# Optimization experiments

Measured on AMD Instinct MI355X. Metric: run time of the kernel, lower is better.

## Reference

```python
import math
import jax, jax.numpy as jnp
import numpy as np

EMBED_DIM = 128
NUM_HEADS = 2
B, N = 4096, 32  # batch of fully-connected ally graphs, N allies each (self-edges included)


def sparsemax(z, axis):
    """Sparsemax (Martins & Astudillo 2016) along `axis`."""
    K = z.shape[axis]
    z_sorted = -jnp.sort(-z, axis=axis)  # descending
    z_cumsum = jnp.cumsum(z_sorted, axis=axis)
    shape = [1] * z.ndim
    shape[axis] = K
    k = jnp.arange(1, K + 1, dtype=z.dtype).reshape(shape)
    support = (1.0 + k * z_sorted) > z_cumsum
    k_sup = jnp.sum(support.astype(z.dtype), axis=axis, keepdims=True)
    tau = (jnp.sum(jnp.where(support, z_sorted, 0.0), axis=axis, keepdims=True) - 1.0) / k_sup
    return jnp.maximum(z - tau, 0.0)


def setup_inputs() -> dict:
    key = jax.random.key(0)
    k1, k2, k3, k4 = jax.random.split(key, 4)
    D, H = EMBED_DIM, NUM_HEADS
    node_feature = jax.random.normal(k1, (B, N, D), dtype=jnp.float32)
    scale = 1.0 / math.sqrt(D)
    WK = jax.random.normal(k2, (D, H * D), dtype=jnp.float32) * scale
    WV = jax.random.normal(k3, (D, H * D), dtype=jnp.float32) * scale
    WQ = jax.random.normal(k4, (D, H * D), dtype=jnp.float32) * scale
    return {"node_feature": node_feature, "WK": WK, "WV": WV, "WQ": WQ}


def reference(node_feature, WK, WV, WQ):
    D, H = EMBED_DIM, NUM_HEADS
    x = node_feature  # [B, N, D]
    # per-node projections; Linear(D, H*D) reshaped to (H, D) as in torch .view
    k = (x @ WK).reshape(B, N, H, D)
    v = (x @ WV).reshape(B, N, H, D)
    q = (x @ WQ).reshape(B, N, H, D)
    # fully connected graph: node i attends over mailbox of all nodes j in same graph
    score = jnp.einsum("bihd,bjhd->bijh", q, k) / math.sqrt(D * H)  # [B, N(i), N(j), H]
    w = sparsemax(score, axis=2)  # sparsemax over neighbor (mailbox) dim
    out = jnp.einsum("bijh,bjhd->bihd", w, v)  # weighted reduction
    out = out.mean(axis=2)  # mean over heads -> [B, N, D]
    output = out.reshape(B * N, D)
    # weight padded to max_num_allies (= N here, so no extra padding needed)
    weight = w.reshape(B * N, N, H)
    return output, weight
```

## Files before the change

### kernel.cpp

```cpp
#include <hip/hip_runtime.h>
#include <hip/hip_bf16.h>


#define NG 4096

typedef short bf16x8 __attribute__((ext_vector_type(8)));
typedef float f32x4 __attribute__((ext_vector_type(4)));

__device__ inline short f2bf(float f) {
    __hip_bfloat16 h = __float2bfloat16(f);
    return __builtin_bit_cast(short, h);
}
__device__ inline unsigned pack2(float a, float b) {
    return (unsigned)(unsigned short)f2bf(a) | ((unsigned)(unsigned short)f2bf(b) << 16);
}

__global__ void pack_m_kernel(const float* __restrict__ WQ, const float* __restrict__ WK,
                              short* __restrict__ packed_m) {
    int idx  = blockIdx.x * 256 + threadIdx.x;
    int jj   = idx & 7;
    int lane = (idx >> 3) & 63;
    int s    = (idx >> 9) & 3;
    int mt   = (idx >> 11) & 15;
    int h    = mt >> 3;
    int a    = s * 32 + (lane >> 4) * 8 + jj;
    int bl   = (mt & 7) * 16 + (lane & 15);
    const float4* qa = (const float4*)(WQ + a * 256 + h * 128);
    const float4* kb = (const float4*)(WK + bl * 256 + h * 128);
    float acc = 0.f;
    #pragma unroll 8
    for (int c = 0; c < 32; ++c) {
        float4 q4 = qa[c], k4 = kb[c];
        acc += q4.x * k4.x + q4.y * k4.y + q4.z * k4.z + q4.w * k4.w;
    }
    packed_m[idx] = f2bf(acc * 0.0625f);
}

__global__ void pack_v_kernel(const float* __restrict__ WV, short* __restrict__ packed_v) {
    int idx  = blockIdx.x * 256 + threadIdx.x;
    int jj   = idx & 7;
    int lane = (idx >> 3) & 63;
    int s    = (idx >> 9) & 3;
    int t    = (idx >> 11) & 15;
    int krow = s * 32 + (lane >> 4) * 8 + jj;
    int col  = t * 16 + (lane & 15);
    packed_v[idx] = f2bf(WV[krow * 256 + col]);
}

__global__ __launch_bounds__(256, 3)
void fused_attn_kernel(const float* __restrict__ x, const short* __restrict__ pm,
                       const short* __restrict__ pv, float* __restrict__ out,
                       float* __restrict__ wgt) {
    __shared__ char __align__(16) smem[46592];
    short* t_s  = (short*)smem;
    short* vT_s = (short*)(smem + 16896);
    float* s_s  = (float*)(smem + 37376);

    int b    = blockIdx.x;
    int tid  = threadIdx.x;
    int lane = tid & 63;
    int wave = tid >> 6;
    int lrow = lane & 15;
    int quad = lane >> 4;

    bf16x8 xf[2][4];
    const float* xg = x + (size_t)b * 4096;
    #pragma unroll
    for (int nt = 0; nt < 2; ++nt)
        #pragma unroll
        for (int s = 0; s < 4; ++s) {
            const float* p0 = &xg[(nt * 16 + lrow) * 128 + s * 32 + quad * 8];
            float4 f0 = *(const float4*)p0;
            float4 f1 = *(const float4*)(p0 + 4);
            bf16x8 v;
            v[0]=f2bf(f0.x); v[1]=f2bf(f0.y); v[2]=f2bf(f0.z); v[3]=f2bf(f0.w);
            v[4]=f2bf(f1.x); v[5]=f2bf(f1.y); v[6]=f2bf(f1.z); v[7]=f2bf(f1.w);
            xf[nt][s] = v;
        }

    #pragma unroll
    for (int t = 0; t < 4; ++t) {
        int mt = wave * 4 + t;
        const short* pb = pm + (mt * 4) * 512 + lane * 8;
        bf16x8 wf[4];
        #pragma unroll
        for (int s = 0; s < 4; ++s) wf[s] = *(const bf16x8*)&pb[s * 512];
        f32x4 acc[2] = {{0.f,0.f,0.f,0.f},{0.f,0.f,0.f,0.f}};
        #pragma unroll
        for (int nt = 0; nt < 2; ++nt)
            #pragma unroll
            for (int s = 0; s < 4; ++s)
                acc[nt] = __builtin_amdgcn_mfma_f32_16x16x32_bf16(wf[s], xf[nt][s], acc[nt], 0, 0, 0);
        #pragma unroll
        for (int nt = 0; nt < 2; ++nt) {
            int addr = (nt * 16 + lrow) * 264 + mt * 16 + quad * 4;
            uint2 pk; pk.x = pack2(acc[nt][0], acc[nt][1]); pk.y = pack2(acc[nt][2], acc[nt][3]);
            *(uint2*)&t_s[addr] = pk;
        }
    }
    #pragma unroll
    for (int t = 0; t < 4; ++t) {
        int ntv = wave * 4 + t;
        const short* pb = pv + (ntv * 4) * 512 + lane * 8;
        bf16x8 wf[4];
        #pragma unroll
        for (int s = 0; s < 4; ++s) wf[s] = *(const bf16x8*)&pb[s * 512];
        f32x4 acc[2] = {{0.f,0.f,0.f,0.f},{0.f,0.f,0.f,0.f}};
        #pragma unroll
        for (int mt = 0; mt < 2; ++mt)
            #pragma unroll
            for (int s = 0; s < 4; ++s)
                acc[mt] = __builtin_amdgcn_mfma_f32_16x16x32_bf16(xf[mt][s], wf[s], acc[mt], 0, 0, 0);
        #pragma unroll
        for (int mt = 0; mt < 2; ++mt) {
            int addr = (ntv * 16 + lrow) * 40 + mt * 16 + quad * 4;
            uint2 pk; pk.x = pack2(acc[mt][0], acc[mt][1]); pk.y = pack2(acc[mt][2], acc[mt][3]);
            *(uint2*)&vT_s[addr] = pk;
        }
    }
    __syncthreads();

    #pragma unroll
    for (int tt = 0; tt < 2; ++tt) {
        int ti = wave * 2 + tt;
        int h = ti >> 2, it = (ti >> 1) & 1, jt = ti & 1;
        f32x4 acc = {0.f, 0.f, 0.f, 0.f};
        #pragma unroll
        for (int s = 0; s < 4; ++s) {
            bf16x8 at = *(const bf16x8*)&t_s[(it * 16 + lrow) * 264 + h * 128 + s * 32 + quad * 8];
            acc = __builtin_amdgcn_mfma_f32_16x16x32_bf16(at, xf[jt][s], acc, 0, 0, 0);
        }
        #pragma unroll
        for (int r = 0; r < 4; ++r)
            s_s[(h * 32 + it * 16 + quad * 4 + r) * 36 + jt * 16 + lrow] = acc[r];
    }
    __syncthreads();

    {
        int j  = lane & 31;
        int hh = lane >> 5;
        #pragma unroll
        for (int ii = 0; ii < 8; ++ii) {
            int i   = wave * 8 + ii;
            int row = hh * 32 + i;
            const float* zr = &s_s[row * 36];
            float z[32];
            #pragma unroll
            for (int c = 0; c < 8; ++c) {
                float4 f = *(const float4*)&zr[c * 4];
                z[c*4] = f.x; z[c*4+1] = f.y; z[c*4+2] = f.z; z[c*4+3] = f.w;
            }
            float zj = zr[j];
            float c0 = 0.f, c1 = 0.f, s0 = 0.f, s1 = 0.f;
            #pragma unroll
            for (int l = 0; l < 32; l += 2) {
                bool g0 = z[l]     > zj;
                bool g1 = z[l + 1] > zj;
                c0 += g0 ? 1.f : 0.f;  s0 += g0 ? z[l]     : 0.f;
                c1 += g1 ? 1.f : 0.f;  s1 += g1 ? z[l + 1] : 0.f;
            }
            float rk  = c0 + c1 + 1.f;
            float cum = s0 + s1 + zj;
            float tc  = (cum - 1.f) / rk;
            #pragma unroll
            for (int m = 1; m <= 16; m <<= 1) tc = fmaxf(tc, __shfl_xor(tc, m, 32));
            float w = fmaxf(zj - tc, 0.f);
            ((short*)zr)[j] = f2bf(w);
            float wo = __shfl_xor(w, 32);
            if (lane < 32) {
                float2 v; v.x = w; v.y = wo;
                *(float2*)&wgt[((size_t)b * 32 + i) * 64 + j * 2] = v;
            }
        }
    }
    __syncthreads();

    #pragma unroll
    for (int tt = 0; tt < 4; ++tt) {
        int ti = wave * 4 + tt;
        int it = ti >> 3, dt = ti & 7;
        f32x4 acc = {0.f, 0.f, 0.f, 0.f};
        #pragma unroll
        for (int h = 0; h < 2; ++h) {
            bf16x8 aw = *(const bf16x8*)((short*)&s_s[(h * 32 + it * 16 + lrow) * 36] + quad * 8);
            bf16x8 bv = *(const bf16x8*)&vT_s[(h * 128 + dt * 16 + lrow) * 40 + quad * 8];
            acc = __builtin_amdgcn_mfma_f32_16x16x32_bf16(aw, bv, acc, 0, 0, 0);
        }
        #pragma unroll
        for (int r = 0; r < 4; ++r)
            out[((size_t)b * 32 + it * 16 + quad * 4 + r) * 128 + dt * 16 + lrow] = acc[r] * 0.5f;
    }
}

extern "C" void kernel_launch(void* const* d_in, const int* in_sizes, int n_in,
                              void* d_out, int out_size, void* d_ws, size_t ws_size,
                              hipStream_t stream) {
    const float* x  = (const float*)d_in[0];
    const float* WK = (const float*)d_in[1];
    const float* WV = (const float*)d_in[2];
    const float* WQ = (const float*)d_in[3];
    float* out = (float*)d_out;
    float* wgt = out + (size_t)NG * 32 * 128;
    short* pm = (short*)d_ws;
    short* pv = pm + 32768;

    hipLaunchKernelGGL(pack_m_kernel, dim3(128), dim3(256), 0, stream, WQ, WK, pm);
    hipLaunchKernelGGL(pack_v_kernel, dim3(128), dim3(256), 0, stream, WV, pv);
    hipLaunchKernelGGL(fused_attn_kernel, dim3(NG), dim3(256), 0, stream, x, pm, pv, out, wgt);
}
```

Measured before the change: 205.8 us.

## Alias score buffer onto projection smem to raise occupancy, merge pack kernels

The score buffer now reuses the shared-memory region of the t projection buffer. An extra barrier and register staging of the score accumulators make this aliasing safe. Shared memory per block drops from about 46KB to 37KB, and launch bounds move from 3 to 4 blocks per SIMD so more workgroups can be resident. The two weight-pack kernels are merged into one launch, and the sparsemax mask-sum now uses an FMA. The costs are one extra barrier per block and possible register pressure under the tighter launch bound.

```diff
diff --git a/kernel.cpp b/kernel.cpp
--- a/kernel.cpp
+++ b/kernel.cpp
@@ -15,46 +15,48 @@
     return (unsigned)(unsigned short)f2bf(a) | ((unsigned)(unsigned short)f2bf(b) << 16);
 }
 
-__global__ void pack_m_kernel(const float* __restrict__ WQ, const float* __restrict__ WK,
-                              short* __restrict__ packed_m) {
-    int idx  = blockIdx.x * 256 + threadIdx.x;
-    int jj   = idx & 7;
-    int lane = (idx >> 3) & 63;
-    int s    = (idx >> 9) & 3;
-    int mt   = (idx >> 11) & 15;
-    int h    = mt >> 3;
-    int a    = s * 32 + (lane >> 4) * 8 + jj;
-    int bl   = (mt & 7) * 16 + (lane & 15);
-    const float4* qa = (const float4*)(WQ + a * 256 + h * 128);
-    const float4* kb = (const float4*)(WK + bl * 256 + h * 128);
-    float acc = 0.f;
-    #pragma unroll 8
-    for (int c = 0; c < 32; ++c) {
-        float4 q4 = qa[c], k4 = kb[c];
-        acc += q4.x * k4.x + q4.y * k4.y + q4.z * k4.z + q4.w * k4.w;
-    }
-    packed_m[idx] = f2bf(acc * 0.0625f);
-}
-
-__global__ void pack_v_kernel(const float* __restrict__ WV, short* __restrict__ packed_v) {
-    int idx  = blockIdx.x * 256 + threadIdx.x;
-    int jj   = idx & 7;
-    int lane = (idx >> 3) & 63;
-    int s    = (idx >> 9) & 3;
-    int t    = (idx >> 11) & 15;
-    int krow = s * 32 + (lane >> 4) * 8 + jj;
-    int col  = t * 16 + (lane & 15);
-    packed_v[idx] = f2bf(WV[krow * 256 + col]);
-}
-
-__global__ __launch_bounds__(256, 3)
+__global__ void pack_mv_kernel(const float* __restrict__ WQ, const float* __restrict__ WK,
+                               const float* __restrict__ WV,
+                               short* __restrict__ pm, short* __restrict__ pv) {
+    int gidx = blockIdx.x * 256 + threadIdx.x;
+    if (gidx < 32768) {
+        int idx  = gidx;
+        int jj   = idx & 7;
+        int lane = (idx >> 3) & 63;
+        int s    = (idx >> 9) & 3;
+        int mt   = (idx >> 11) & 15;
+        int h    = mt >> 3;
+        int a    = s * 32 + (lane >> 4) * 8 + jj;
+        int bl   = (mt & 7) * 16 + (lane & 15);
+        const float4* qa = (const float4*)(WQ + a * 256 + h * 128);
+        const float4* kb = (const float4*)(WK + bl * 256 + h * 128);
+        float acc = 0.f;
+        #pragma unroll 8
+        for (int c = 0; c < 32; ++c) {
+            float4 q4 = qa[c], k4 = kb[c];
+            acc += q4.x * k4.x + q4.y * k4.y + q4.z * k4.z + q4.w * k4.w;
+        }
+        pm[idx] = f2bf(acc * 0.0625f);
+    } else {
+        int idx  = gidx - 32768;
+        int jj   = idx & 7;
+        int lane = (idx >> 3) & 63;
+        int s    = (idx >> 9) & 3;
+        int t    = (idx >> 11) & 15;
+        int krow = s * 32 + (lane >> 4) * 8 + jj;
+        int col  = t * 16 + (lane & 15);
+        pv[idx] = f2bf(WV[krow * 256 + col]);
+    }
+}
+
+__global__ __launch_bounds__(256, 4)
 void fused_attn_kernel(const float* __restrict__ x, const short* __restrict__ pm,
                        const short* __restrict__ pv, float* __restrict__ out,
                        float* __restrict__ wgt) {
-    __shared__ char __align__(16) smem[46592];
+    __shared__ char __align__(16) smem[37376];
     short* t_s  = (short*)smem;
+    float* s_s  = (float*)smem;
     short* vT_s = (short*)(smem + 16896);
-    float* s_s  = (float*)(smem + 37376);
 
     int b    = blockIdx.x;
     int tid  = threadIdx.x;
@@ -120,6 +122,7 @@
     }
     __syncthreads();
 
+    f32x4 sacc[2];
     #pragma unroll
     for (int tt = 0; tt < 2; ++tt) {
         int ti = wave * 2 + tt;
@@ -130,9 +133,17 @@
             bf16x8 at = *(const bf16x8*)&t_s[(it * 16 + lrow) * 264 + h * 128 + s * 32 + quad * 8];
             acc = __builtin_amdgcn_mfma_f32_16x16x32_bf16(at, xf[jt][s], acc, 0, 0, 0);
         }
+        sacc[tt] = acc;
+    }
+    __syncthreads();
+
+    #pragma unroll
+    for (int tt = 0; tt < 2; ++tt) {
+        int ti = wave * 2 + tt;
+        int h = ti >> 2, it = (ti >> 1) & 1, jt = ti & 1;
         #pragma unroll
         for (int r = 0; r < 4; ++r)
-            s_s[(h * 32 + it * 16 + quad * 4 + r) * 36 + jt * 16 + lrow] = acc[r];
+            s_s[(h * 32 + it * 16 + quad * 4 + r) * 36 + jt * 16 + lrow] = sacc[tt][r];
     }
     __syncthreads();
 
@@ -154,10 +165,10 @@
             float c0 = 0.f, c1 = 0.f, s0 = 0.f, s1 = 0.f;
             #pragma unroll
             for (int l = 0; l < 32; l += 2) {
-                bool g0 = z[l]     > zj;
-                bool g1 = z[l + 1] > zj;
-                c0 += g0 ? 1.f : 0.f;  s0 += g0 ? z[l]     : 0.f;
-                c1 += g1 ? 1.f : 0.f;  s1 += g1 ? z[l + 1] : 0.f;
+                float m0 = (z[l]     > zj) ? 1.f : 0.f;
+                float m1 = (z[l + 1] > zj) ? 1.f : 0.f;
+                c0 += m0;  s0 = __builtin_fmaf(m0, z[l],     s0);
+                c1 += m1;  s1 = __builtin_fmaf(m1, z[l + 1], s1);
             }
             float rk  = c0 + c1 + 1.f;
             float cum = s0 + s1 + zj;
@@ -204,7 +215,6 @@
     short* pm = (short*)d_ws;
     short* pv = pm + 32768;
 
-    hipLaunchKernelGGL(pack_m_kernel, dim3(128), dim3(256), 0, stream, WQ, WK, pm);
-    hipLaunchKernelGGL(pack_v_kernel, dim3(128), dim3(256), 0, stream, WV, pv);
+    hipLaunchKernelGGL(pack_mv_kernel, dim3(256), dim3(256), 0, stream, WQ, WK, WV, pm, pv);
     hipLaunchKernelGGL(fused_attn_kernel, dim3(NG), dim3(256), 0, stream, x, pm, pv, out, wgt);
 }
```

New measurement: 201.8 us. -2.0%, faster.
